# Kernel optimization log

Measured on AMD Instinct MI355X. Metric: run time of the kernel, lower is better.

The kernel has to match this reference:

```python
import math
import jax, jax.numpy as jnp
import numpy as np

B, CIN, COUT, H, W, K, SDIM = 8, 32, 32, 512, 512, 3, 512


def setup_inputs() -> dict:
    key = jax.random.key(0)
    k1, k2, k3, k4 = jax.random.split(key, 4)
    return {
        "x": jax.random.normal(k1, (B, CIN, H, W), dtype=jnp.float32),
        "style": jax.random.normal(k2, (B, SDIM), dtype=jnp.float32),
        "weight": jax.random.normal(k3, (1, COUT, CIN, K, K), dtype=jnp.float32),
        "mod_w": jax.random.normal(k4, (CIN, SDIM), dtype=jnp.float32),
        "mod_b": jnp.zeros((CIN,), dtype=jnp.float32),
    }


def reference(x, style, weight, mod_w, mod_b):
    # x: [B, Cin, H, W]; style: [B, S]; weight: [1, Cout, Cin, K, K]
    b, cin, h, w = x.shape
    _, cout, _, k, _ = weight.shape
    sdim = mod_w.shape[1]

    # EqualLinear modulation: out = style @ (W * scale)^T + bias * lr_mul (lr_mul=1)
    mod_scale = 1.0 / math.sqrt(sdim)
    s = style @ (mod_w * mod_scale).T + mod_b  # [B, Cin]

    # Per-sample weight modulation + demodulation
    conv_scale = 1.0 / math.sqrt(cin * k * k)
    wmod = conv_scale * weight * s[:, None, :, None, None]  # [B, Cout, Cin, K, K]
    demod = jax.lax.rsqrt(jnp.sum(wmod * wmod, axis=(2, 3, 4)) + 1e-8)  # [B, Cout]
    wmod = wmod * demod[:, :, None, None, None]

    pad = k // 2

    def conv_one(xi, wi):
        # xi: [Cin, H, W], wi: [Cout, Cin, K, K]
        return jax.lax.conv_general_dilated(
            xi[None], wi, window_strides=(1, 1),
            padding=[(pad, pad), (pad, pad)],
            dimension_numbers=("NCHW", "OIHW", "NCHW"),
        )[0]

    out = jax.vmap(conv_one)(x, wmod)  # [B, Cout, H, W]
    return out
```

## Files before the change

### kernel.cpp

```cpp
#include <hip/hip_runtime.h>

#define B_    8
#define CIN   32
#define COUT  32
#define H_    512
#define W_    512
#define SDIM  512

#define MOD_SCALE  0.044194173824159216f
#define CONV_SCALE 0.05892556509887896f

#define PXB 128
#define LW  130

typedef unsigned short u16;
typedef __attribute__((ext_vector_type(8))) short           bf16x8;
typedef __attribute__((ext_vector_type(8))) unsigned short  ushort8;
typedef __attribute__((ext_vector_type(4))) float           f32x4;

__device__ __forceinline__ u16 f2bf(float x) {
    union { float f; unsigned u; } v; v.f = x;
    unsigned r = v.u + 0x7FFFu + ((v.u >> 16) & 1u);
    return (u16)(r >> 16);
}
__device__ __forceinline__ float bf2f(u16 h) {
    union { float f; unsigned u; } v; v.u = ((unsigned)h) << 16;
    return v.f;
}

__global__ __launch_bounds__(64) void modweights_kernel(
    const float* __restrict__ style,
    const float* __restrict__ weight,
    const float* __restrict__ mod_w,
    const float* __restrict__ mod_b,
    u16* __restrict__ wh,
    u16* __restrict__ wl)
{
    const int b  = blockIdx.x / COUT;
    const int co = blockIdx.x % COUT;
    const int t  = threadIdx.x;

    __shared__ float s_sh[CIN];

    const float4* st4 = (const float4*)(style + (size_t)b * SDIM);
    const float4 sv0 = st4[t];
    const float4 sv1 = st4[t + 64];

    for (int ci = 0; ci < CIN; ++ci) {
        const float4* mw4 = (const float4*)(mod_w + (size_t)ci * SDIM);
        const float4 a = mw4[t];
        const float4 c = mw4[t + 64];
        float p = sv0.x*a.x + sv0.y*a.y + sv0.z*a.z + sv0.w*a.w
                + sv1.x*c.x + sv1.y*c.y + sv1.z*c.z + sv1.w*c.w;
        #pragma unroll
        for (int off = 32; off > 0; off >>= 1) p += __shfl_xor(p, off);
        if (t == 0) s_sh[ci] = p * MOD_SCALE + mod_b[ci];
    }
    __syncthreads();

    const float* wco = weight + (size_t)co * CIN * 9;

    float ss = 0.f;
    for (int i = t; i < CIN * 9; i += 64) {
        const float v = CONV_SCALE * wco[i] * s_sh[i / 9];
        ss += v * v;
    }
    #pragma unroll
    for (int off = 32; off > 0; off >>= 1) ss += __shfl_xor(ss, off);
    const float dem = rsqrtf(ss + 1e-8f);

    for (int i = t; i < CIN * 9; i += 64) {
        const int ci  = i / 9;
        const int ofs = i - ci * 9;
        const float v = CONV_SCALE * wco[i] * s_sh[ci] * dem;
        const size_t o = (((size_t)b * 9 + ofs) * COUT + co) * CIN + ci;
        const u16 hb = f2bf(v);
        wh[o] = hb;
        wl[o] = f2bf(v - bf2f(hb));
    }
}

__global__ __launch_bounds__(256) void conv_kernel(
    const float* __restrict__ x,
    const u16* __restrict__ wh,
    const u16* __restrict__ wl,
    float* __restrict__ out)
{
    __shared__ u16 xh[3 * LW * CIN];
    __shared__ u16 xl[3 * LW * CIN];

    const int t  = threadIdx.x;
    const int w0 = blockIdx.x * PXB;
    const int h  = blockIdx.y;
    const int b  = blockIdx.z;

    const int lane = t & 63;
    const int wid  = t >> 6;
    const int wm   = wid >> 1;
    const int wn   = wid & 1;
    const int l15  = lane & 15;
    const int k0   = (lane >> 4) * 8;

    bf16x8 ah[9], al[9];
    #pragma unroll
    for (int ofs = 0; ofs < 9; ++ofs) {
        const size_t o = (((size_t)b * 9 + ofs) * COUT + wm * 16 + l15) * CIN + k0;
        ah[ofs] = *(const bf16x8*)(wh + o);
        al[ofs] = *(const bf16x8*)(wl + o);
    }

    for (int task = t; task < 3 * 4 * LW; task += 256) {
        const int w  = task % LW;
        const int rc = task / LW;
        const int r  = rc >> 2;
        const int cg = rc & 3;
        const int gw = w0 + w - 1;
        const int ih = h + r - 1;
        float v[8];
        if (ih >= 0 && ih < H_ && gw >= 0 && gw < W_) {
            const float* p = x + ((size_t)(b * CIN + cg * 8) * H_ + ih) * W_ + gw;
            #pragma unroll
            for (int j = 0; j < 8; ++j) v[j] = p[(size_t)j * H_ * W_];
        } else {
            #pragma unroll
            for (int j = 0; j < 8; ++j) v[j] = 0.f;
        }
        ushort8 hv, lv;
        #pragma unroll
        for (int j = 0; j < 8; ++j) {
            const u16 hb = f2bf(v[j]);
            hv[j] = hb;
            lv[j] = f2bf(v[j] - bf2f(hb));
        }
        const int idx = (((r * LW + w) * CIN) + cg * 8) ^ ((w & 7) << 3);
        *(ushort8*)(xh + idx) = hv;
        *(ushort8*)(xl + idx) = lv;
    }
    __syncthreads();

    f32x4 acc[4];
    #pragma unroll
    for (int sub = 0; sub < 4; ++sub) acc[sub] = (f32x4){0.f, 0.f, 0.f, 0.f};

    #pragma unroll
    for (int ofs = 0; ofs < 9; ++ofs) {
        const int kh = ofs / 3;
        const int kw = ofs - kh * 3;
        #pragma unroll
        for (int sub = 0; sub < 4; ++sub) {
            const int wlp = wn * 64 + sub * 16 + l15 + kw;
            const int idx = (((kh * LW + wlp) * CIN) + k0) ^ ((wlp & 7) << 3);
            const bf16x8 bh = *(const bf16x8*)(xh + idx);
            const bf16x8 bl = *(const bf16x8*)(xl + idx);
            acc[sub] = __builtin_amdgcn_mfma_f32_16x16x32_bf16(ah[ofs], bh, acc[sub], 0, 0, 0);
            acc[sub] = __builtin_amdgcn_mfma_f32_16x16x32_bf16(ah[ofs], bl, acc[sub], 0, 0, 0);
            acc[sub] = __builtin_amdgcn_mfma_f32_16x16x32_bf16(al[ofs], bh, acc[sub], 0, 0, 0);
        }
    }

    #pragma unroll
    for (int sub = 0; sub < 4; ++sub) {
        const int opx = w0 + wn * 64 + sub * 16 + l15;
        #pragma unroll
        for (int j = 0; j < 4; ++j) {
            const int oco = wm * 16 + (lane >> 4) * 4 + j;
            out[(((size_t)b * COUT + oco) * H_ + h) * W_ + opx] = acc[sub][j];
        }
    }
}

extern "C" void kernel_launch(void* const* d_in, const int* in_sizes, int n_in,
                              void* d_out, int out_size, void* d_ws, size_t ws_size,
                              hipStream_t stream)
{
    const float* x      = (const float*)d_in[0];
    const float* style  = (const float*)d_in[1];
    const float* weight = (const float*)d_in[2];
    const float* mod_w  = (const float*)d_in[3];
    const float* mod_b  = (const float*)d_in[4];
    float* out = (float*)d_out;

    u16* wh = (u16*)d_ws;
    u16* wl = wh + (size_t)B_ * 9 * COUT * CIN;

    modweights_kernel<<<B_ * COUT, 64, 0, stream>>>(style, weight, mod_w, mod_b, wh, wl);

    dim3 grid(W_ / PXB, H_, B_);
    conv_kernel<<<grid, 256, 0, stream>>>(x, wh, wl, out);
}
```

Measured before the change: 593.9 us.

## Compute four output rows per block to reuse input halo rows

Each conv block now covers 4 output rows by 64 pixels, loading 6 input rows into shared memory instead of 3 rows for a single output row. Each shared-memory B fragment is reused across up to three output rows, which cuts redundant global loads and hi/lo bf16 splitting of the halo. The cost is more accumulator registers and a narrower width tile, with more column halo overhead per pixel.

```diff
diff --git a/kernel.cpp b/kernel.cpp
--- a/kernel.cpp
+++ b/kernel.cpp
@@ -10,12 +10,13 @@
 #define MOD_SCALE  0.044194173824159216f
 #define CONV_SCALE 0.05892556509887896f
 
-#define PXB 128
-#define LW  130
+#define PXB 64
+#define RB  4
+#define LR  6
+#define LW  66
 
 typedef unsigned short u16;
 typedef __attribute__((ext_vector_type(8))) short           bf16x8;
-typedef __attribute__((ext_vector_type(8))) unsigned short  ushort8;
 typedef __attribute__((ext_vector_type(4))) float           f32x4;
 
 __device__ __forceinline__ u16 f2bf(float x) {
@@ -86,12 +87,12 @@
     const u16* __restrict__ wl,
     float* __restrict__ out)
 {
-    __shared__ u16 xh[3 * LW * CIN];
-    __shared__ u16 xl[3 * LW * CIN];
+    __shared__ u16 xh[LR * LW * CIN];
+    __shared__ u16 xl[LR * LW * CIN];
 
     const int t  = threadIdx.x;
     const int w0 = blockIdx.x * PXB;
-    const int h  = blockIdx.y;
+    const int h0 = blockIdx.y * RB;
     const int b  = blockIdx.z;
 
     const int lane = t & 63;
@@ -109,15 +110,15 @@
         al[ofs] = *(const bf16x8*)(wl + o);
     }
 
-    for (int task = t; task < 3 * 4 * LW; task += 256) {
+    for (int task = t; task < LR * 4 * LW; task += 256) {
         const int w  = task % LW;
         const int rc = task / LW;
         const int r  = rc >> 2;
         const int cg = rc & 3;
         const int gw = w0 + w - 1;
-        const int ih = h + r - 1;
+        const int ih = h0 + r - 1;
         float v[8];
-        if (ih >= 0 && ih < H_ && gw >= 0 && gw < W_) {
+        if ((unsigned)ih < (unsigned)H_ && (unsigned)gw < (unsigned)W_) {
             const float* p = x + ((size_t)(b * CIN + cg * 8) * H_ + ih) * W_ + gw;
             #pragma unroll
             for (int j = 0; j < 8; ++j) v[j] = p[(size_t)j * H_ * W_];
@@ -125,46 +126,69 @@
             #pragma unroll
             for (int j = 0; j < 8; ++j) v[j] = 0.f;
         }
-        ushort8 hv, lv;
-        #pragma unroll
-        for (int j = 0; j < 8; ++j) {
-            const u16 hb = f2bf(v[j]);
-            hv[j] = hb;
-            lv[j] = f2bf(v[j] - bf2f(hb));
+        unsigned hu[4], lu[4];
+        #pragma unroll
+        for (int q = 0; q < 4; ++q) {
+            const u16 h0b = f2bf(v[2*q]);
+            const u16 h1b = f2bf(v[2*q+1]);
+            const u16 l0b = f2bf(v[2*q]   - bf2f(h0b));
+            const u16 l1b = f2bf(v[2*q+1] - bf2f(h1b));
+            hu[q] = (unsigned)h0b | ((unsigned)h1b << 16);
+            lu[q] = (unsigned)l0b | ((unsigned)l1b << 16);
         }
         const int idx = (((r * LW + w) * CIN) + cg * 8) ^ ((w & 7) << 3);
-        *(ushort8*)(xh + idx) = hv;
-        *(ushort8*)(xl + idx) = lv;
+        *(uint4*)(xh + idx) = make_uint4(hu[0], hu[1], hu[2], hu[3]);
+        *(uint4*)(xl + idx) = make_uint4(lu[0], lu[1], lu[2], lu[3]);
     }
     __syncthreads();
 
-    f32x4 acc[4];
-    #pragma unroll
-    for (int sub = 0; sub < 4; ++sub) acc[sub] = (f32x4){0.f, 0.f, 0.f, 0.f};
-
-    #pragma unroll
-    for (int ofs = 0; ofs < 9; ++ofs) {
-        const int kh = ofs / 3;
-        const int kw = ofs - kh * 3;
-        #pragma unroll
-        for (int sub = 0; sub < 4; ++sub) {
-            const int wlp = wn * 64 + sub * 16 + l15 + kw;
-            const int idx = (((kh * LW + wlp) * CIN) + k0) ^ ((wlp & 7) << 3);
-            const bf16x8 bh = *(const bf16x8*)(xh + idx);
-            const bf16x8 bl = *(const bf16x8*)(xl + idx);
-            acc[sub] = __builtin_amdgcn_mfma_f32_16x16x32_bf16(ah[ofs], bh, acc[sub], 0, 0, 0);
-            acc[sub] = __builtin_amdgcn_mfma_f32_16x16x32_bf16(ah[ofs], bl, acc[sub], 0, 0, 0);
-            acc[sub] = __builtin_amdgcn_mfma_f32_16x16x32_bf16(al[ofs], bh, acc[sub], 0, 0, 0);
-        }
-    }
-
-    #pragma unroll
-    for (int sub = 0; sub < 4; ++sub) {
-        const int opx = w0 + wn * 64 + sub * 16 + l15;
-        #pragma unroll
-        for (int j = 0; j < 4; ++j) {
-            const int oco = wm * 16 + (lane >> 4) * 4 + j;
-            out[(((size_t)b * COUT + oco) * H_ + h) * W_ + opx] = acc[sub][j];
+    f32x4 acc[RB][2];
+    #pragma unroll
+    for (int r = 0; r < RB; ++r) {
+        acc[r][0] = (f32x4){0.f, 0.f, 0.f, 0.f};
+        acc[r][1] = (f32x4){0.f, 0.f, 0.f, 0.f};
+    }
+
+    #pragma unroll
+    for (int r_in = 0; r_in < LR; ++r_in) {
+        #pragma unroll
+        for (int sub = 0; sub < 2; ++sub) {
+            bf16x8 bh[3], bl[3];
+            #pragma unroll
+            for (int kw = 0; kw < 3; ++kw) {
+                const int wl_ = wn * 32 + sub * 16 + l15 + kw;
+                const int idx = (((r_in * LW + wl_) * CIN) + k0) ^ ((wl_ & 7) << 3);
+                bh[kw] = *(const bf16x8*)(xh + idx);
+                bl[kw] = *(const bf16x8*)(xl + idx);
+            }
+            #pragma unroll
+            for (int kh = 0; kh < 3; ++kh) {
+                const int r_out = r_in - kh;
+                if (r_out < 0 || r_out >= RB) continue;
+                #pragma unroll
+                for (int kw = 0; kw < 3; ++kw) {
+                    const int tap = kh * 3 + kw;
+                    acc[r_out][sub] = __builtin_amdgcn_mfma_f32_16x16x32_bf16(
+                        ah[tap], bh[kw], acc[r_out][sub], 0, 0, 0);
+                    acc[r_out][sub] = __builtin_amdgcn_mfma_f32_16x16x32_bf16(
+                        ah[tap], bl[kw], acc[r_out][sub], 0, 0, 0);
+                    acc[r_out][sub] = __builtin_amdgcn_mfma_f32_16x16x32_bf16(
+                        al[tap], bh[kw], acc[r_out][sub], 0, 0, 0);
+                }
+            }
+        }
+    }
+
+    #pragma unroll
+    for (int r = 0; r < RB; ++r) {
+        #pragma unroll
+        for (int sub = 0; sub < 2; ++sub) {
+            const int opx = w0 + wn * 32 + sub * 16 + l15;
+            #pragma unroll
+            for (int j = 0; j < 4; ++j) {
+                const int oco = wm * 16 + (lane >> 4) * 4 + j;
+                out[(((size_t)b * COUT + oco) * H_ + h0 + r) * W_ + opx] = acc[r][sub][j];
+            }
         }
     }
 }
@@ -185,6 +209,6 @@
 
     modweights_kernel<<<B_ * COUT, 64, 0, stream>>>(style, weight, mod_w, mod_b, wh, wl);
 
-    dim3 grid(W_ / PXB, H_, B_);
+    dim3 grid(W_ / PXB, H_ / RB, B_);
     conv_kernel<<<grid, 256, 0, stream>>>(x, wh, wl, out);
 }
```

After: 531.1 us. -10.6%, faster.
